# Optimization experiments

Hardware: AMD Instinct MI355X
Metric: run time of the kernel (lower is better)

The kernel has to match this reference:

```python
import jax, jax.numpy as jnp
import numpy as np

N = 524288
H = 128
NB = 55  # number of bones


def setup_inputs() -> dict:
    key = jax.random.key(0)
    ks = jax.random.split(key, 8)
    xyz = jax.random.normal(ks[0], (N, 3), dtype=jnp.float32)
    quats = jax.random.normal(ks[1], (N, 4), dtype=jnp.float32)
    # bone transforms: identity-ish affine 4x4 per bone
    tfs = jnp.eye(4, dtype=jnp.float32)[None] + 0.05 * jax.random.normal(ks[2], (NB, 4, 4), dtype=jnp.float32)
    aabb_min = -4.0 * jnp.ones(3, dtype=jnp.float32)
    aabb_max = 4.0 * jnp.ones(3, dtype=jnp.float32)
    W0 = jax.random.normal(ks[3], (3, H), dtype=jnp.float32) / np.sqrt(3.0)
    b0 = jnp.zeros(H, dtype=jnp.float32)
    W1 = jax.random.normal(ks[4], (H, H), dtype=jnp.float32) / np.sqrt(H)
    b1 = jnp.zeros(H, dtype=jnp.float32)
    W2 = jax.random.normal(ks[5], (H, H), dtype=jnp.float32) / np.sqrt(H)
    b2 = jnp.zeros(H, dtype=jnp.float32)
    W3 = jax.random.normal(ks[6], (H, 59), dtype=jnp.float32) / np.sqrt(H)
    b3 = jnp.zeros(59, dtype=jnp.float32)
    return dict(xyz=xyz, quats=quats, tfs=tfs, aabb_min=aabb_min, aabb_max=aabb_max,
                W0=W0, b0=b0, W1=W1, b1=b1, W2=W2, b2=b2, W3=W3, b3=b3)


def hierarchical_softmax(x):
    # x: (N, 59) logits -> (N, 55) probabilities over SMPL-X bones
    s = jax.nn.sigmoid(x)

    def sm(cols):
        return jax.nn.softmax(x[:, cols], axis=-1)

    p = jnp.ones((x.shape[0], NB), x.dtype)

    def branch(p, parent, child):
        parent = np.array(parent); child = np.array(child)
        a = p[:, parent]
        p = p.at[:, child].set(a * s[:, child])
        return p.at[:, parent].set(a * (1.0 - s[:, child]))

    def subtree(p, parent, gate, children):
        children = np.array(children)
        a = p[:, parent][:, None]
        g = s[:, gate][:, None]
        p = p.at[:, children].set(a * g * sm(children))
        return p.at[:, parent].set(a[:, 0] * (1.0 - s[:, gate]))

    c123 = np.array([1, 2, 3])
    p = p.at[:, c123].set(s[:, 0:1] * sm(c123))
    p = p.at[:, 0].set(1.0 - s[:, 0])
    p = branch(p, [1, 2, 3], [4, 5, 6])
    p = branch(p, [4, 5, 6], [7, 8, 9])
    p = branch(p, [7, 8], [10, 11])
    p = subtree(p, 9, 55, [12, 13, 14])
    p = branch(p, [12], [15])
    p = branch(p, [13, 14], [16, 17])
    p = branch(p, [16, 17], [18, 19])
    p = branch(p, [18, 19], [20, 21])
    p = subtree(p, 15, 56, [22, 23, 24])
    p = subtree(p, 20, 57, [25, 28, 31, 34, 37])
    p = subtree(p, 21, 58, [40, 43, 46, 49, 52])
    p = branch(p, [25, 28, 31, 34, 37], [26, 29, 32, 35, 38])
    p = branch(p, [26, 29, 32, 35, 38], [27, 30, 33, 36, 39])
    p = branch(p, [40, 43, 46, 49, 52], [41, 44, 47, 50, 53])
    p = branch(p, [41, 44, 47, 50, 53], [42, 45, 48, 51, 54])
    return p


def build_rotation(q):
    # quaternion (w, x, y, z) -> rotation matrix, gaussian-splatting convention
    q = q / jnp.linalg.norm(q, axis=-1, keepdims=True)
    r, x, y, z = q[:, 0], q[:, 1], q[:, 2], q[:, 3]
    R = jnp.stack([
        1 - 2 * (y * y + z * z), 2 * (x * y - r * z), 2 * (x * z + r * y),
        2 * (x * y + r * z), 1 - 2 * (x * x + z * z), 2 * (y * z - r * x),
        2 * (x * z - r * y), 2 * (y * z + r * x), 1 - 2 * (x * x + y * y),
    ], axis=-1).reshape(-1, 3, 3)
    return R


def mat_to_quat(R):
    # robust matrix -> quaternion (w, x, y, z), vectorized branch selection
    m00, m01, m02 = R[:, 0, 0], R[:, 0, 1], R[:, 0, 2]
    m10, m11, m12 = R[:, 1, 0], R[:, 1, 1], R[:, 1, 2]
    m20, m21, m22 = R[:, 2, 0], R[:, 2, 1], R[:, 2, 2]
    t0 = 1 + m00 + m11 + m22
    t1 = 1 + m00 - m11 - m22
    t2 = 1 - m00 + m11 - m22
    t3 = 1 - m00 - m11 + m22
    q0 = jnp.stack([t0, m21 - m12, m02 - m20, m10 - m01], -1)
    q1 = jnp.stack([m21 - m12, t1, m01 + m10, m02 + m20], -1)
    q2 = jnp.stack([m02 - m20, m01 + m10, t2, m12 + m21], -1)
    q3 = jnp.stack([m10 - m01, m02 + m20, m12 + m21, t3], -1)
    t = jnp.stack([t0, t1, t2, t3], -1)                      # (N,4)
    qs = jnp.stack([q0, q1, q2, q3], 1)                      # (N,4,4)
    scale = 0.5 * jax.lax.rsqrt(jnp.maximum(t, 1e-8))
    qs = qs * scale[..., None]
    best = jnp.argmax(t, axis=-1)
    q = jnp.take_along_axis(qs, best[:, None, None], axis=1)[:, 0]
    return q / jnp.linalg.norm(q, axis=-1, keepdims=True)


def reference(xyz, quats, tfs, aabb_min, aabb_max, W0, b0, W1, b1, W2, b2, W3, b3):
    # aabb.normalize(xyz, sym=True)
    xyz_norm = 2.0 * (xyz - aabb_min) / (aabb_max - aabb_min) - 1.0
    # lbs_network: softplus MLP 3 -> H -> H -> H -> 59
    h = jax.nn.softplus(xyz_norm @ W0 + b0)
    h = jax.nn.softplus(h @ W1 + b1)
    h = jax.nn.softplus(h @ W2 + b2)
    logits = h @ W3 + b3                                     # (N,59)
    pts_W = hierarchical_softmax(logits)                     # (N,55)
    # blend bone transforms
    T_fwd = (pts_W @ tfs.reshape(NB, 16)).reshape(-1, 4, 4)  # (N,4,4)
    # transform points (homogeneous)
    homo = jnp.concatenate([xyz, jnp.ones((xyz.shape[0], 1), xyz.dtype)], -1)
    x_bar = jnp.einsum('nij,nj->ni', T_fwd, homo)[:, :3]
    # transform rotations
    rot_hat = build_rotation(quats)
    rot_bar = jnp.einsum('nij,njk->nik', T_fwd[:, :3, :3], rot_hat)
    quat_bar = mat_to_quat(rot_bar)
    return x_bar, rot_bar, quat_bar, T_fwd
```

## Files before the change

### kernel.cpp

```cpp
#include <hip/hip_runtime.h>
#include <hip/hip_bf16.h>
#include <math.h>

#define NPTS 524288
#define H 128
#define NB 55
#define NL 59
#define BLK 256
#define ROWB 528

typedef __attribute__((ext_vector_type(8))) short short8;
typedef __attribute__((ext_vector_type(4))) short short4v;
typedef __attribute__((ext_vector_type(4))) float float4v;

#define WS_TFHI  0
#define WS_B3P   2048
#define WS_W1HI  4096
#define WS_W1LO  36864
#define WS_W2HI  69632
#define WS_W2LO  102400
#define WS_W3HI  135168
#define WS_W3LO  151552
#define WS_TFLO  167936

__device__ __forceinline__ float fast_rcp(float x) { return __builtin_amdgcn_rcpf(x); }
__device__ __forceinline__ float fast_rsq(float x) { return __builtin_amdgcn_rsqf(x); }

#define LOG2E 1.44269504f
#define LN2   0.69314718f

__device__ __forceinline__ float sp_act(float x) {
    float e = __builtin_amdgcn_exp2f(x * LOG2E);
    return LN2 * __builtin_amdgcn_logf(1.0f + e);
}
__device__ __forceinline__ float sigf(float x) {
    float e = __builtin_amdgcn_exp2f(-x * LOG2E);
    return fast_rcp(1.0f + e);
}
__device__ __forceinline__ unsigned f2u(float f) { union { float f; unsigned u; } v; v.f = f; return v.u; }
__device__ __forceinline__ float u2f(unsigned u) { union { unsigned u; float f; } v; v.u = u; return v.f; }
__device__ __forceinline__ void split_bf(float v, short& hi, short& lo) {
    unsigned uh = (f2u(v) + 0x8000u) & 0xFFFF0000u;
    hi = (short)(uh >> 16);
    float r = v - u2f(uh);
    lo = (short)((f2u(r) + 0x8000u) >> 16);
}
__device__ __forceinline__ float4v mfma16(short8 a, short8 b, float4v c) {
    return __builtin_amdgcn_mfma_f32_16x16x32_bf16(a, b, c, 0, 0, 0);
}

__global__ void prep_kernel(const float* __restrict__ W1, const float* __restrict__ W2,
                            const float* __restrict__ W3, const float* __restrict__ b3,
                            const float* __restrict__ tfs, char* __restrict__ ws)
{
    const int tid = blockIdx.x * blockDim.x + threadIdx.x;
    {
        const int n = tid >> 7, k = tid & 127;
        short hi, lo;
        split_bf(W1[k * H + n], hi, lo);
        ((short*)(ws + WS_W1HI))[n * H + k] = hi;
        ((short*)(ws + WS_W1LO))[n * H + k] = lo;
        split_bf(W2[k * H + n], hi, lo);
        ((short*)(ws + WS_W2HI))[n * H + k] = hi;
        ((short*)(ws + WS_W2LO))[n * H + k] = lo;
    }
    if (tid < 64 * 128) {
        const int n = tid >> 7, k = tid & 127;
        float w = (n < NL) ? W3[k * NL + n] : 0.0f;
        short hi, lo;
        split_bf(w, hi, lo);
        ((short*)(ws + WS_W3HI))[n * H + k] = hi;
        ((short*)(ws + WS_W3LO))[n * H + k] = lo;
    }
    if (tid < 16 * 64) {
        const int e = tid >> 6, b = tid & 63;
        float w = (b < NB) ? tfs[b * 16 + e] : 0.0f;
        short hi, lo;
        split_bf(w, hi, lo);
        ((short*)(ws + WS_TFHI))[e * 64 + b] = hi;
        ((short*)(ws + WS_TFLO))[e * 64 + b] = lo;
    }
    if (tid < 64) {
        ((float*)(ws + WS_B3P))[tid] = (tid < NL) ? b3[tid] : 0.0f;
    }
}

template<int NFT, bool SOFTPLUS>
__device__ __forceinline__ void mfma_layer(char* lds, int mrow0, int lane,
                                           const short* __restrict__ Whi,
                                           const short* __restrict__ Wlo,
                                           const float* __restrict__ bias)
{
    const int l15 = lane & 15;
    const int g = lane >> 4;
    float4v acc[NFT][4];
#pragma unroll
    for (int ft = 0; ft < NFT; ++ft) {
        float4v bv = *(const float4v*)(bias + ft * 16 + g * 4);
#pragma unroll
        for (int pt = 0; pt < 4; ++pt) acc[ft][pt] = bv;
    }
#pragma unroll
    for (int k0 = 0; k0 < 128; k0 += 32) {
        short8 Bhi[4], Blo[4];
#pragma unroll
        for (int pt = 0; pt < 4; ++pt) {
            const char* rowp = lds + (mrow0 + pt * 16 + l15) * ROWB;
            Bhi[pt] = *(const short8*)(rowp + 2 * k0 + 16 * g);
            Blo[pt] = *(const short8*)(rowp + 256 + 2 * k0 + 16 * g);
        }
#pragma unroll
        for (int ft = 0; ft < NFT; ++ft) {
            short8 Ahi = *(const short8*)(Whi + (ft * 16 + l15) * H + k0 + g * 8);
            short8 Alo = *(const short8*)(Wlo + (ft * 16 + l15) * H + k0 + g * 8);
#pragma unroll
            for (int pt = 0; pt < 4; ++pt) {
                acc[ft][pt] = mfma16(Ahi, Bhi[pt], acc[ft][pt]);
                acc[ft][pt] = mfma16(Ahi, Blo[pt], acc[ft][pt]);
                acc[ft][pt] = mfma16(Alo, Bhi[pt], acc[ft][pt]);
            }
        }
    }
#pragma unroll
    for (int ft = 0; ft < NFT; ++ft) {
#pragma unroll
        for (int pt = 0; pt < 4; ++pt) {
            char* rowp = lds + (mrow0 + pt * 16 + l15) * ROWB;
            if constexpr (SOFTPLUS) {
                short4v whi, wlo;
                short h0, h1, h2, h3, l0, l1, l2, l3;
                split_bf(sp_act(acc[ft][pt].x), h0, l0);
                split_bf(sp_act(acc[ft][pt].y), h1, l1);
                split_bf(sp_act(acc[ft][pt].z), h2, l2);
                split_bf(sp_act(acc[ft][pt].w), h3, l3);
                whi.x = h0; whi.y = h1; whi.z = h2; whi.w = h3;
                wlo.x = l0; wlo.y = l1; wlo.z = l2; wlo.w = l3;
                *(short4v*)(rowp + (ft * 16 + g * 4) * 2) = whi;
                *(short4v*)(rowp + 256 + (ft * 16 + g * 4) * 2) = wlo;
            } else {
                *(float4v*)(rowp + (ft * 16 + g * 4) * 4) = acc[ft][pt];
            }
        }
    }
}

__global__ void __launch_bounds__(BLK, 1)
skin_kernel(const float* __restrict__ xyz, const float* __restrict__ quats,
            const float* __restrict__ amn, const float* __restrict__ amx,
            const float* __restrict__ W0, const float* __restrict__ b0,
            const float* __restrict__ b1, const float* __restrict__ b2,
            const char* __restrict__ ws, float* __restrict__ out)
{
    __shared__ __align__(16) char lds[BLK * ROWB];
    const int tid = threadIdx.x;
    const int lane = tid & 63;
    const int wv = tid >> 6;
    const int l15 = lane & 15;
    const int g = lane >> 4;
    const int mrow0 = wv * 64;
    const int n = blockIdx.x * BLK + tid;

    const float x = xyz[3 * n + 0];
    const float y = xyz[3 * n + 1];
    const float z = xyz[3 * n + 2];
    {
        const float xn = 2.0f * (x - amn[0]) / (amx[0] - amn[0]) - 1.0f;
        const float yn = 2.0f * (y - amn[1]) / (amx[1] - amn[1]) - 1.0f;
        const float zn = 2.0f * (z - amn[2]) / (amx[2] - amn[2]) - 1.0f;
        char* row = lds + tid * ROWB;
#pragma unroll
        for (int jj = 0; jj < H; jj += 8) {
            short8 hp, lp;
#pragma unroll
            for (int u = 0; u < 8; ++u) {
                const int j = jj + u;
                float a = fmaf(zn, W0[2 * H + j], fmaf(yn, W0[H + j], fmaf(xn, W0[j], b0[j])));
                float h = sp_act(a);
                short hi, lo;
                split_bf(h, hi, lo);
                hp[u] = hi; lp[u] = lo;
            }
            *(short8*)(row + 2 * jj) = hp;
            *(short8*)(row + 256 + 2 * jj) = lp;
        }
    }

    mfma_layer<8, true>(lds, mrow0, lane, (const short*)(ws + WS_W1HI),
                        (const short*)(ws + WS_W1LO), b1);
    mfma_layer<8, true>(lds, mrow0, lane, (const short*)(ws + WS_W2HI),
                        (const short*)(ws + WS_W2LO), b2);
    mfma_layer<4, false>(lds, mrow0, lane, (const short*)(ws + WS_W3HI),
                         (const short*)(ws + WS_W3LO), (const float*)(ws + WS_B3P));

    float l[64];
#pragma unroll
    for (int j = 0; j < 16; ++j)
        *(float4v*)&l[4 * j] = *(const float4v*)(lds + tid * ROWB + 16 * j);

    float p[NB];
#define BR(par, ch)                                         \
    do {                                                    \
        float a_ = p[par];                                  \
        float s_ = sigf(l[ch]);                             \
        p[ch] = a_ * s_;                                    \
        p[par] = a_ * (1.0f - s_);                          \
    } while (0)
#define SUB3(par, gt, c0, c1, c2)                                            \
    do {                                                                     \
        float a_ = p[par];                                                   \
        float g_ = sigf(l[gt]);                                              \
        float m_ = fmaxf(l[c0], fmaxf(l[c1], l[c2]));                        \
        float e0_ = __expf(l[c0] - m_);                                      \
        float e1_ = __expf(l[c1] - m_);                                      \
        float e2_ = __expf(l[c2] - m_);                                      \
        float inv_ = a_ * g_ * fast_rcp(e0_ + e1_ + e2_);                    \
        p[c0] = e0_ * inv_;                                                  \
        p[c1] = e1_ * inv_;                                                  \
        p[c2] = e2_ * inv_;                                                  \
        p[par] = a_ * (1.0f - g_);                                           \
    } while (0)
#define SUB5(par, gt, c0, c1, c2, c3, c4)                                    \
    do {                                                                     \
        float a_ = p[par];                                                   \
        float g_ = sigf(l[gt]);                                              \
        float m_ = fmaxf(fmaxf(fmaxf(l[c0], l[c1]), fmaxf(l[c2], l[c3])), l[c4]); \
        float e0_ = __expf(l[c0] - m_);                                      \
        float e1_ = __expf(l[c1] - m_);                                      \
        float e2_ = __expf(l[c2] - m_);                                      \
        float e3_ = __expf(l[c3] - m_);                                      \
        float e4_ = __expf(l[c4] - m_);                                      \
        float inv_ = a_ * g_ * fast_rcp(e0_ + e1_ + e2_ + e3_ + e4_);        \
        p[c0] = e0_ * inv_;                                                  \
        p[c1] = e1_ * inv_;                                                  \
        p[c2] = e2_ * inv_;                                                  \
        p[c3] = e3_ * inv_;                                                  \
        p[c4] = e4_ * inv_;                                                  \
        p[par] = a_ * (1.0f - g_);                                           \
    } while (0)

    {
        float s0_ = sigf(l[0]);
        float m_ = fmaxf(l[1], fmaxf(l[2], l[3]));
        float e1_ = __expf(l[1] - m_);
        float e2_ = __expf(l[2] - m_);
        float e3_ = __expf(l[3] - m_);
        float inv_ = s0_ * fast_rcp(e1_ + e2_ + e3_);
        p[1] = e1_ * inv_;
        p[2] = e2_ * inv_;
        p[3] = e3_ * inv_;
        p[0] = 1.0f - s0_;
    }
    BR(1, 4); BR(2, 5); BR(3, 6);
    BR(4, 7); BR(5, 8); BR(6, 9);
    BR(7, 10); BR(8, 11);
    SUB3(9, 55, 12, 13, 14);
    BR(12, 15);
    BR(13, 16); BR(14, 17);
    BR(16, 18); BR(17, 19);
    BR(18, 20); BR(19, 21);
    SUB3(15, 56, 22, 23, 24);
    SUB5(20, 57, 25, 28, 31, 34, 37);
    SUB5(21, 58, 40, 43, 46, 49, 52);
    BR(25, 26); BR(28, 29); BR(31, 32); BR(34, 35); BR(37, 38);
    BR(26, 27); BR(29, 30); BR(32, 33); BR(35, 36); BR(38, 39);
    BR(40, 41); BR(43, 44); BR(46, 47); BR(49, 50); BR(52, 53);
    BR(41, 42); BR(44, 45); BR(47, 48); BR(50, 51); BR(53, 54);

    {
        char* row = lds + tid * ROWB;
#pragma unroll
        for (int jj = 0; jj < 64; jj += 8) {
            short8 hp, lp;
#pragma unroll
            for (int u = 0; u < 8; ++u) {
                const int b = jj + u;
                float v = (b < NB) ? p[b] : 0.0f;
                short hi, lo;
                split_bf(v, hi, lo);
                hp[u] = hi; lp[u] = lo;
            }
            *(short8*)(row + 2 * jj) = hp;
            *(short8*)(row + 128 + 2 * jj) = lp;
        }
    }
    {
        const short* Ahi_p = (const short*)(ws + WS_TFHI);
        const short* Alo_p = (const short*)(ws + WS_TFLO);
        float4v acc[4];
#pragma unroll
        for (int pt = 0; pt < 4; ++pt) acc[pt] = (float4v){0.f, 0.f, 0.f, 0.f};
#pragma unroll
        for (int k0 = 0; k0 < 64; k0 += 32) {
            short8 Bhi[4], Blo[4];
#pragma unroll
            for (int pt = 0; pt < 4; ++pt) {
                const char* rowp = lds + (mrow0 + pt * 16 + l15) * ROWB;
                Bhi[pt] = *(const short8*)(rowp + 2 * k0 + 16 * g);
                Blo[pt] = *(const short8*)(rowp + 128 + 2 * k0 + 16 * g);
            }
            short8 Ahi = *(const short8*)(Ahi_p + l15 * 64 + k0 + g * 8);
            short8 Alo = *(const short8*)(Alo_p + l15 * 64 + k0 + g * 8);
#pragma unroll
            for (int pt = 0; pt < 4; ++pt) {
                acc[pt] = mfma16(Ahi, Bhi[pt], acc[pt]);
                acc[pt] = mfma16(Ahi, Blo[pt], acc[pt]);
                acc[pt] = mfma16(Alo, Bhi[pt], acc[pt]);
            }
        }
#pragma unroll
        for (int pt = 0; pt < 4; ++pt)
            *(float4v*)(lds + (mrow0 + pt * 16 + l15) * ROWB + 256 + g * 16) = acc[pt];
    }
    float T[16];
#pragma unroll
    for (int j = 0; j < 4; ++j)
        *(float4v*)&T[4 * j] = *(const float4v*)(lds + tid * ROWB + 256 + 16 * j);

    const float xb0 = fmaf(T[0], x, fmaf(T[1], y, fmaf(T[2], z, T[3])));
    const float xb1 = fmaf(T[4], x, fmaf(T[5], y, fmaf(T[6], z, T[7])));
    const float xb2 = fmaf(T[8], x, fmaf(T[9], y, fmaf(T[10], z, T[11])));

    float qr = quats[4 * n + 0];
    float qx = quats[4 * n + 1];
    float qy = quats[4 * n + 2];
    float qz = quats[4 * n + 3];
    {
        float inv = fast_rsq(qr * qr + qx * qx + qy * qy + qz * qz);
        qr *= inv; qx *= inv; qy *= inv; qz *= inv;
    }
    const float R00 = 1.0f - 2.0f * (qy * qy + qz * qz);
    const float R01 = 2.0f * (qx * qy - qr * qz);
    const float R02 = 2.0f * (qx * qz + qr * qy);
    const float R10 = 2.0f * (qx * qy + qr * qz);
    const float R11 = 1.0f - 2.0f * (qx * qx + qz * qz);
    const float R12 = 2.0f * (qy * qz - qr * qx);
    const float R20 = 2.0f * (qx * qz - qr * qy);
    const float R21 = 2.0f * (qy * qz + qr * qx);
    const float R22 = 1.0f - 2.0f * (qx * qx + qy * qy);

    const float B00 = T[0] * R00 + T[1] * R10 + T[2] * R20;
    const float B01 = T[0] * R01 + T[1] * R11 + T[2] * R21;
    const float B02 = T[0] * R02 + T[1] * R12 + T[2] * R22;
    const float B10 = T[4] * R00 + T[5] * R10 + T[6] * R20;
    const float B11 = T[4] * R01 + T[5] * R11 + T[6] * R21;
    const float B12 = T[4] * R02 + T[5] * R12 + T[6] * R22;
    const float B20 = T[8] * R00 + T[9] * R10 + T[10] * R20;
    const float B21 = T[8] * R01 + T[9] * R11 + T[10] * R21;
    const float B22 = T[8] * R02 + T[9] * R12 + T[10] * R22;

    const float t0 = 1.0f + B00 + B11 + B22;
    const float t1 = 1.0f + B00 - B11 - B22;
    const float t2 = 1.0f - B00 + B11 - B22;
    const float t3 = 1.0f - B00 - B11 + B22;
    const float s0 = 0.5f * fast_rsq(fmaxf(t0, 1e-8f));
    const float s1 = 0.5f * fast_rsq(fmaxf(t1, 1e-8f));
    const float s2 = 0.5f * fast_rsq(fmaxf(t2, 1e-8f));
    const float s3 = 0.5f * fast_rsq(fmaxf(t3, 1e-8f));
    const float q0w = t0 * s0, q0x = (B21 - B12) * s0, q0y = (B02 - B20) * s0, q0z = (B10 - B01) * s0;
    const float q1w = (B21 - B12) * s1, q1x = t1 * s1, q1y = (B01 + B10) * s1, q1z = (B02 + B20) * s1;
    const float q2w = (B02 - B20) * s2, q2x = (B01 + B10) * s2, q2y = t2 * s2, q2z = (B12 + B21) * s2;
    const float q3w = (B10 - B01) * s3, q3x = (B02 + B20) * s3, q3y = (B12 + B21) * s3, q3z = t3 * s3;

    int best = 0;
    float tb = t0;
    if (t1 > tb) { best = 1; tb = t1; }
    if (t2 > tb) { best = 2; tb = t2; }
    if (t3 > tb) { best = 3; tb = t3; }

    float Qw = (best == 0) ? q0w : (best == 1) ? q1w : (best == 2) ? q2w : q3w;
    float Qx = (best == 0) ? q0x : (best == 1) ? q1x : (best == 2) ? q2x : q3x;
    float Qy = (best == 0) ? q0y : (best == 1) ? q1y : (best == 2) ? q2y : q3y;
    float Qz = (best == 0) ? q0z : (best == 1) ? q1z : (best == 2) ? q2z : q3z;
    {
        float inv = fast_rsq(Qw * Qw + Qx * Qx + Qy * Qy + Qz * Qz);
        Qw *= inv; Qx *= inv; Qy *= inv; Qz *= inv;
    }

    out[3 * n + 0] = xb0;
    out[3 * n + 1] = xb1;
    out[3 * n + 2] = xb2;
    float* rb = out + 3 * (size_t)NPTS;
    rb[9 * n + 0] = B00; rb[9 * n + 1] = B01; rb[9 * n + 2] = B02;
    rb[9 * n + 3] = B10; rb[9 * n + 4] = B11; rb[9 * n + 5] = B12;
    rb[9 * n + 6] = B20; rb[9 * n + 7] = B21; rb[9 * n + 8] = B22;
    float4* qb = (float4*)(out + 12 * (size_t)NPTS);
    qb[n] = make_float4(Qw, Qx, Qy, Qz);
    float4* tf = (float4*)(out + 16 * (size_t)NPTS);
    tf[4 * n + 0] = make_float4(T[0], T[1], T[2], T[3]);
    tf[4 * n + 1] = make_float4(T[4], T[5], T[6], T[7]);
    tf[4 * n + 2] = make_float4(T[8], T[9], T[10], T[11]);
    tf[4 * n + 3] = make_float4(T[12], T[13], T[14], T[15]);
}

extern "C" void kernel_launch(void* const* d_in, const int* in_sizes, int n_in,
                              void* d_out, int out_size, void* d_ws, size_t ws_size,
                              hipStream_t stream) {
    const float* xyz = (const float*)d_in[0];
    const float* quats = (const float*)d_in[1];
    const float* tfs = (const float*)d_in[2];
    const float* amn = (const float*)d_in[3];
    const float* amx = (const float*)d_in[4];
    const float* W0 = (const float*)d_in[5];
    const float* b0 = (const float*)d_in[6];
    const float* W1 = (const float*)d_in[7];
    const float* b1 = (const float*)d_in[8];
    const float* W2 = (const float*)d_in[9];
    const float* b2 = (const float*)d_in[10];
    const float* W3 = (const float*)d_in[11];
    const float* b3 = (const float*)d_in[12];
    float* out = (float*)d_out;
    char* ws = (char*)d_ws;

    hipLaunchKernelGGL(prep_kernel, dim3(64), dim3(256), 0, stream, W1, W2, W3, b3, tfs, ws);
    hipLaunchKernelGGL(skin_kernel, dim3(NPTS / BLK), dim3(BLK), 0, stream,
                       xyz, quats, amn, amx, W0, b0, b1, b2, (const char*)ws, out);
}
```

Baseline: 338.6 us.

## Move layer-0 onto MFMA and fold softplus log2/ln2 scaling into weights

The first MLP layer (3->128) now runs as a bf16 hi/lo split MFMA with K padded to 32, using a pre-packed W0 in the workspace, instead of a scalar per-thread FMA loop with 128 softplus evaluations per thread. The softplus is kept in the log2 domain: LOG2E is folded into W0 and the biases, and LN2 into W3, which removes the per-element multiplies. Packing of bf16 hi/lo pairs uses perm instructions and 8-byte stores. The cost is extra MFMA issue and LDS traffic for layer 0, plus small rounding differences from the rescaled weights.

Result: no change. 332.9 us (-1.7%).

```diff
diff --git a/kernel.cpp b/kernel.cpp
--- a/kernel.cpp
+++ b/kernel.cpp
@@ -10,8 +10,8 @@
 #define ROWB 528
 
 typedef __attribute__((ext_vector_type(8))) short short8;
-typedef __attribute__((ext_vector_type(4))) short short4v;
 typedef __attribute__((ext_vector_type(4))) float float4v;
+typedef __attribute__((ext_vector_type(2))) unsigned uint2v;
 
 #define WS_TFHI  0
 #define WS_B3P   2048
@@ -22,20 +22,18 @@
 #define WS_W3HI  135168
 #define WS_W3LO  151552
 #define WS_TFLO  167936
+#define WS_W0P   169984
+
+#define LOG2E 1.44269504f
+#define LN2   0.69314718f
 
 __device__ __forceinline__ float fast_rcp(float x) { return __builtin_amdgcn_rcpf(x); }
 __device__ __forceinline__ float fast_rsq(float x) { return __builtin_amdgcn_rsqf(x); }
-
-#define LOG2E 1.44269504f
-#define LN2   0.69314718f
-
-__device__ __forceinline__ float sp_act(float x) {
-    float e = __builtin_amdgcn_exp2f(x * LOG2E);
-    return LN2 * __builtin_amdgcn_logf(1.0f + e);
+__device__ __forceinline__ float sp_log2(float x) {
+    return __builtin_amdgcn_logf(1.0f + __builtin_amdgcn_exp2f(x));
 }
 __device__ __forceinline__ float sigf(float x) {
-    float e = __builtin_amdgcn_exp2f(-x * LOG2E);
-    return fast_rcp(1.0f + e);
+    return fast_rcp(1.0f + __builtin_amdgcn_exp2f(-x * LOG2E));
 }
 __device__ __forceinline__ unsigned f2u(float f) { union { float f; unsigned u; } v; v.f = f; return v.u; }
 __device__ __forceinline__ float u2f(unsigned u) { union { unsigned u; float f; } v; v.u = u; return v.f; }
@@ -45,13 +43,21 @@
     float r = v - u2f(uh);
     lo = (short)((f2u(r) + 0x8000u) >> 16);
 }
+__device__ __forceinline__ void pack2_hl(float a, float b, unsigned& hw, unsigned& lw) {
+    unsigned ua = f2u(a) + 0x8000u, ub = f2u(b) + 0x8000u;
+    hw = __builtin_amdgcn_perm(ub, ua, 0x07060302u);
+    float ra = a - u2f(ua & 0xFFFF0000u);
+    float rb = b - u2f(ub & 0xFFFF0000u);
+    lw = __builtin_amdgcn_perm(f2u(rb) + 0x8000u, f2u(ra) + 0x8000u, 0x07060302u);
+}
 __device__ __forceinline__ float4v mfma16(short8 a, short8 b, float4v c) {
     return __builtin_amdgcn_mfma_f32_16x16x32_bf16(a, b, c, 0, 0, 0);
 }
 
-__global__ void prep_kernel(const float* __restrict__ W1, const float* __restrict__ W2,
-                            const float* __restrict__ W3, const float* __restrict__ b3,
-                            const float* __restrict__ tfs, char* __restrict__ ws)
+__global__ void prep_kernel(const float* __restrict__ W0, const float* __restrict__ W1,
+                            const float* __restrict__ W2, const float* __restrict__ W3,
+                            const float* __restrict__ b3, const float* __restrict__ tfs,
+                            char* __restrict__ ws)
 {
     const int tid = blockIdx.x * blockDim.x + threadIdx.x;
     {
@@ -66,7 +72,7 @@
     }
     if (tid < 64 * 128) {
         const int n = tid >> 7, k = tid & 127;
-        float w = (n < NL) ? W3[k * NL + n] : 0.0f;
+        float w = (n < NL) ? W3[k * NL + n] * LN2 : 0.0f;
         short hi, lo;
         split_bf(w, hi, lo);
         ((short*)(ws + WS_W3HI))[n * H + k] = hi;
@@ -80,6 +86,17 @@
         ((short*)(ws + WS_TFHI))[e * 64 + b] = hi;
         ((short*)(ws + WS_TFLO))[e * 64 + b] = lo;
     }
+    if (tid < 128 * 32) {
+        const int n = tid >> 5, k = tid & 31;
+        short s = 0;
+        if (k < 9) {
+            const int kk = (k < 3) ? k : ((k < 6) ? k - 3 : k - 6);
+            short hi, lo;
+            split_bf(W0[kk * H + n] * LOG2E, hi, lo);
+            s = (k < 6) ? hi : lo;
+        }
+        ((short*)(ws + WS_W0P))[n * 32 + k] = s;
+    }
     if (tid < 64) {
         ((float*)(ws + WS_B3P))[tid] = (tid < NL) ? b3[tid] : 0.0f;
     }
@@ -89,7 +106,7 @@
 __device__ __forceinline__ void mfma_layer(char* lds, int mrow0, int lane,
                                            const short* __restrict__ Whi,
                                            const short* __restrict__ Wlo,
-                                           const float* __restrict__ bias)
+                                           const float* __restrict__ bias, float bscale)
 {
     const int l15 = lane & 15;
     const int g = lane >> 4;
@@ -97,6 +114,7 @@
 #pragma unroll
     for (int ft = 0; ft < NFT; ++ft) {
         float4v bv = *(const float4v*)(bias + ft * 16 + g * 4);
+        bv *= bscale;
 #pragma unroll
         for (int pt = 0; pt < 4; ++pt) acc[ft][pt] = bv;
     }
@@ -127,16 +145,18 @@
         for (int pt = 0; pt < 4; ++pt) {
             char* rowp = lds + (mrow0 + pt * 16 + l15) * ROWB;
             if constexpr (SOFTPLUS) {
-                short4v whi, wlo;
-                short h0, h1, h2, h3, l0, l1, l2, l3;
-                split_bf(sp_act(acc[ft][pt].x), h0, l0);
-                split_bf(sp_act(acc[ft][pt].y), h1, l1);
-                split_bf(sp_act(acc[ft][pt].z), h2, l2);
-                split_bf(sp_act(acc[ft][pt].w), h3, l3);
-                whi.x = h0; whi.y = h1; whi.z = h2; whi.w = h3;
-                wlo.x = l0; wlo.y = l1; wlo.z = l2; wlo.w = l3;
-                *(short4v*)(rowp + (ft * 16 + g * 4) * 2) = whi;
-                *(short4v*)(rowp + 256 + (ft * 16 + g * 4) * 2) = wlo;
+                float s0 = sp_log2(acc[ft][pt].x);
+                float s1 = sp_log2(acc[ft][pt].y);
+                float s2 = sp_log2(acc[ft][pt].z);
+                float s3 = sp_log2(acc[ft][pt].w);
+                unsigned hx, lx, hy, ly;
+                pack2_hl(s0, s1, hx, lx);
+                pack2_hl(s2, s3, hy, ly);
+                uint2v hw, lw;
+                hw.x = hx; hw.y = hy;
+                lw.x = lx; lw.y = ly;
+                *(uint2v*)(rowp + (ft * 16 + g * 4) * 2) = hw;
+                *(uint2v*)(rowp + 256 + (ft * 16 + g * 4) * 2) = lw;
             } else {
                 *(float4v*)(rowp + (ft * 16 + g * 4) * 4) = acc[ft][pt];
             }
@@ -147,9 +167,9 @@
 __global__ void __launch_bounds__(BLK, 1)
 skin_kernel(const float* __restrict__ xyz, const float* __restrict__ quats,
             const float* __restrict__ amn, const float* __restrict__ amx,
-            const float* __restrict__ W0, const float* __restrict__ b0,
-            const float* __restrict__ b1, const float* __restrict__ b2,
-            const char* __restrict__ ws, float* __restrict__ out)
+            const float* __restrict__ b0, const float* __restrict__ b1,
+            const float* __restrict__ b2, const char* __restrict__ ws,
+            float* __restrict__ out)
 {
     __shared__ __align__(16) char lds[BLK * ROWB];
     const int tid = threadIdx.x;
@@ -164,33 +184,72 @@
     const float y = xyz[3 * n + 1];
     const float z = xyz[3 * n + 2];
     {
-        const float xn = 2.0f * (x - amn[0]) / (amx[0] - amn[0]) - 1.0f;
-        const float yn = 2.0f * (y - amn[1]) / (amx[1] - amn[1]) - 1.0f;
-        const float zn = 2.0f * (z - amn[2]) / (amx[2] - amn[2]) - 1.0f;
+        const float xn = 2.0f * (x - amn[0]) * fast_rcp(amx[0] - amn[0]) - 1.0f;
+        const float yn = 2.0f * (y - amn[1]) * fast_rcp(amx[1] - amn[1]) - 1.0f;
+        const float zn = 2.0f * (z - amn[2]) * fast_rcp(amx[2] - amn[2]) - 1.0f;
+        short xh, xl, yh, yl, zh, zl;
+        split_bf(xn, xh, xl);
+        split_bf(yn, yh, yl);
+        split_bf(zn, zh, zl);
+        short8 s0v; short8 zer = {0, 0, 0, 0, 0, 0, 0, 0};
+        s0v[0] = xh; s0v[1] = yh; s0v[2] = zh; s0v[3] = xl;
+        s0v[4] = yl; s0v[5] = zl; s0v[6] = xh; s0v[7] = yh;
+        short8 s1v = zer; s1v[0] = zh;
         char* row = lds + tid * ROWB;
-#pragma unroll
-        for (int jj = 0; jj < H; jj += 8) {
-            short8 hp, lp;
-#pragma unroll
-            for (int u = 0; u < 8; ++u) {
-                const int j = jj + u;
-                float a = fmaf(zn, W0[2 * H + j], fmaf(yn, W0[H + j], fmaf(xn, W0[j], b0[j])));
-                float h = sp_act(a);
-                short hi, lo;
-                split_bf(h, hi, lo);
-                hp[u] = hi; lp[u] = lo;
+        *(short8*)(row) = s0v;
+        *(short8*)(row + 16) = s1v;
+        *(short8*)(row + 32) = zer;
+        *(short8*)(row + 48) = zer;
+    }
+
+    {
+        const short* W0p = (const short*)(ws + WS_W0P);
+        float4v acc[8][4];
+#pragma unroll
+        for (int ft = 0; ft < 8; ++ft) {
+            float4v bv = *(const float4v*)(b0 + ft * 16 + g * 4);
+            bv *= LOG2E;
+#pragma unroll
+            for (int pt = 0; pt < 4; ++pt) acc[ft][pt] = bv;
+        }
+        short8 B[4];
+#pragma unroll
+        for (int pt = 0; pt < 4; ++pt)
+            B[pt] = *(const short8*)(lds + (mrow0 + pt * 16 + l15) * ROWB + 16 * g);
+#pragma unroll
+        for (int ft = 0; ft < 8; ++ft) {
+            short8 A = *(const short8*)(W0p + (ft * 16 + l15) * 32 + g * 8);
+#pragma unroll
+            for (int pt = 0; pt < 4; ++pt)
+                acc[ft][pt] = mfma16(A, B[pt], acc[ft][pt]);
+        }
+#pragma unroll
+        for (int ft = 0; ft < 8; ++ft) {
+#pragma unroll
+            for (int pt = 0; pt < 4; ++pt) {
+                char* rowp = lds + (mrow0 + pt * 16 + l15) * ROWB;
+                float s0 = sp_log2(acc[ft][pt].x);
+                float s1 = sp_log2(acc[ft][pt].y);
+                float s2 = sp_log2(acc[ft][pt].z);
+                float s3 = sp_log2(acc[ft][pt].w);
+                unsigned hx, lx, hy, ly;
+                pack2_hl(s0, s1, hx, lx);
+                pack2_hl(s2, s3, hy, ly);
+                uint2v hw, lw;
+                hw.x = hx; hw.y = hy;
+                lw.x = lx; lw.y = ly;
+                *(uint2v*)(rowp + (ft * 16 + g * 4) * 2) = hw;
+                *(uint2v*)(rowp + 256 + (ft * 16 + g * 4) * 2) = lw;
             }
-            *(short8*)(row + 2 * jj) = hp;
-            *(short8*)(row + 256 + 2 * jj) = lp;
         }
     }
 
     mfma_layer<8, true>(lds, mrow0, lane, (const short*)(ws + WS_W1HI),
-                        (const short*)(ws + WS_W1LO), b1);
+                        (const short*)(ws + WS_W1LO), b1, LOG2E);
     mfma_layer<8, true>(lds, mrow0, lane, (const short*)(ws + WS_W2HI),
-                        (const short*)(ws + WS_W2LO), b2);
+                        (const short*)(ws + WS_W2LO), b2, LOG2E);
     mfma_layer<4, false>(lds, mrow0, lane, (const short*)(ws + WS_W3HI),
-                         (const short*)(ws + WS_W3LO), (const float*)(ws + WS_B3P));
+                         (const short*)(ws + WS_W3LO), (const float*)(ws + WS_B3P), 1.0f);
 
     float l[64];
 #pragma unroll
@@ -269,18 +328,19 @@
     {
         char* row = lds + tid * ROWB;
 #pragma unroll
-        for (int jj = 0; jj < 64; jj += 8) {
-            short8 hp, lp;
-#pragma unroll
-            for (int u = 0; u < 8; ++u) {
-                const int b = jj + u;
-                float v = (b < NB) ? p[b] : 0.0f;
-                short hi, lo;
-                split_bf(v, hi, lo);
-                hp[u] = hi; lp[u] = lo;
-            }
-            *(short8*)(row + 2 * jj) = hp;
-            *(short8*)(row + 128 + 2 * jj) = lp;
+        for (int jj = 0; jj < 64; jj += 4) {
+            float v0 = (jj + 0 < NB) ? p[jj + 0] : 0.0f;
+            float v1 = (jj + 1 < NB) ? p[jj + 1] : 0.0f;
+            float v2 = (jj + 2 < NB) ? p[jj + 2] : 0.0f;
+            float v3 = (jj + 3 < NB) ? p[jj + 3] : 0.0f;
+            unsigned hx, lx, hy, ly;
+            pack2_hl(v0, v1, hx, lx);
+            pack2_hl(v2, v3, hy, ly);
+            uint2v hw, lw;
+            hw.x = hx; hw.y = hy;
+            lw.x = lx; lw.y = ly;
+            *(uint2v*)(row + 2 * jj) = hw;
+            *(uint2v*)(row + 128 + 2 * jj) = lw;
         }
     }
     {
@@ -411,7 +471,7 @@
     float* out = (float*)d_out;
     char* ws = (char*)d_ws;
 
-    hipLaunchKernelGGL(prep_kernel, dim3(64), dim3(256), 0, stream, W1, W2, W3, b3, tfs, ws);
+    hipLaunchKernelGGL(prep_kernel, dim3(64), dim3(256), 0, stream, W0, W1, W2, W3, b3, tfs, ws);
     hipLaunchKernelGGL(skin_kernel, dim3(NPTS / BLK), dim3(BLK), 0, stream,
-                       xyz, quats, amn, amx, W0, b0, b1, b2, (const char*)ws, out);
-}
+                       xyz, quats, amn, amx, b0, b1, b2, (const char*)ws, out);
+}
```
